# Optimization experiments

Measured on AMD Instinct MI355X. Metric: run time of the kernel, lower is better.

## Reference

```python
import jax, jax.numpy as jnp
import numpy as np

N, E, F, H = 50000, 1600000, 128, 128  # nodes, edges, input_nf, hidden_nf


def setup_inputs() -> dict:
    key = jax.random.key(0)
    ks = jax.random.split(key, 16)
    s = 0.05
    inp = {
        "h": jax.random.normal(ks[0], (N, F), jnp.float32),
        "coord": jax.random.normal(ks[1], (N, 3), jnp.float32),
        "edge_index": jax.random.randint(ks[2], (2, E), 0, N, jnp.int32),
        # edge_mlp: Linear(2F+1, H) -> SiLU -> Linear(H, H) -> SiLU
        "We1": jax.random.normal(ks[3], (2 * F + 1, H), jnp.float32) * s,
        "be1": jnp.zeros((H,), jnp.float32),
        "We2": jax.random.normal(ks[4], (H, H), jnp.float32) * s,
        "be2": jnp.zeros((H,), jnp.float32),
        # node_mlp: Linear(H+F, H) -> SiLU -> Linear(H, F)
        "Wn1": jax.random.normal(ks[5], (H + F, H), jnp.float32) * s,
        "bn1": jnp.zeros((H,), jnp.float32),
        "Wn2": jax.random.normal(ks[6], (H, F), jnp.float32) * s,
        "bn2": jnp.zeros((F,), jnp.float32),
        # coord_mlp: Linear(H, H) -> SiLU -> Linear(H, 1, bias=False) (xavier gain 0.001)
        "Wc1": jax.random.normal(ks[7], (H, H), jnp.float32) * s,
        "bc1": jnp.zeros((H,), jnp.float32),
        "Wc2": jax.random.normal(ks[8], (H, 1), jnp.float32) * 0.001,
    }
    return inp


def reference(h, coord, edge_index, We1, be1, We2, be2, Wn1, bn1, Wn2, bn2, Wc1, bc1, Wc2):
    row, col = edge_index[0], edge_index[1]
    n = h.shape[0]

    # coord2radial (normalize=False)
    coord_diff = coord[row] - coord[col]                      # [E, 3]
    radial = jnp.sum(coord_diff * coord_diff, axis=1, keepdims=True)  # [E, 1]

    # edge_model (attention=False, edge_attr=None)
    e_in = jnp.concatenate([h[row], h[col], radial], axis=1)  # [E, 2F+1]
    edge_feat = jax.nn.silu(jax.nn.silu(e_in @ We1 + be1) @ We2 + be2)  # [E, H]

    # coord_model (coords_agg='mean', reflection_equiv=True, tanh=False)
    phi = jax.nn.silu(edge_feat @ Wc1 + bc1) @ Wc2            # [E, 1]
    trans = coord_diff * phi                                   # [E, 3]
    agg_c = jax.ops.segment_sum(trans, row, num_segments=n)    # [N, 3]
    cnt = jax.ops.segment_sum(jnp.ones((trans.shape[0], 1), trans.dtype), row, num_segments=n)
    coord_out = coord + agg_c / jnp.maximum(cnt, 1.0)

    # node_model (node_attr=None, residual=True)
    agg_h = jax.ops.segment_sum(edge_feat, row, num_segments=n)  # [N, H]
    n_in = jnp.concatenate([h, agg_h], axis=1)                   # [N, F+H]
    h_out = h + (jax.nn.silu(n_in @ Wn1 + bn1) @ Wn2 + bn2)

    return h_out, coord_out
```

## Files before the change

### kernel.cpp

```cpp
#include <hip/hip_runtime.h>


typedef float f32x4 __attribute__((ext_vector_type(4)));
typedef short s16x8 __attribute__((ext_vector_type(8)));

#define NN   50000
#define EE   1600000
#define NHF  6400000
#define NBIN 50000
#define NT   25000
#define A1B  782
#define NODB 782

__device__ __forceinline__ unsigned short f2bf(float x){
  union { float f; unsigned int u; } v; v.f = x;
  unsigned int r = v.u + 0x7fffu + ((v.u >> 16) & 1u);
  return (unsigned short)(r >> 16);
}
__device__ __forceinline__ unsigned int pack2(float a, float b){
  unsigned int r;
  asm("v_cvt_pk_bf16_f32 %0, %1, %2" : "=v"(r) : "v"(a), "v"(b));
  return r;
}
__device__ __forceinline__ float silu_f(float x){
  return x * __builtin_amdgcn_rcpf(1.f + __expf(-x));
}
__device__ __forceinline__ float bflo(unsigned int u){ return __uint_as_float(u << 16); }
__device__ __forceinline__ float bfhi(unsigned int u){ return __uint_as_float(u & 0xffff0000u); }

__device__ __forceinline__ f32x4 mfma16(s16x8 a, s16x8 b, f32x4 c){
  return __builtin_amdgcn_mfma_f32_16x16x32_bf16(a, b, c, 0, 0, 0);
}

template<int CTRL> __device__ __forceinline__ float dppf(float x){
  return __int_as_float(__builtin_amdgcn_update_dpp(0, __float_as_int(x), CTRL, 0xF, 0xF, true));
}
template<int CTRL> __device__ __forceinline__ int dppi(int x){
  return __builtin_amdgcn_update_dpp(-1, x, CTRL, 0xF, 0xF, false);
}

__device__ __forceinline__ short* sptr(short* base, int fi, int slot){
  return (short*)((char*)base + (fi << 10) + (((slot << 4) ^ ((fi & 3) << 5))));
}

__global__ void pack_weights(const float* __restrict__ We1, const float* __restrict__ We2,
                             const float* __restrict__ Wc1, const float* __restrict__ Wn1,
                             const float* __restrict__ Wn2, short* __restrict__ wp)
{
  int b = blockIdx.x;
  int m = b >> 5, t = b & 31;
  int ft = t >> 2, ks = t & 3;
  int lane = threadIdx.x;
  const float* src;
  switch (m) {
    case 0: src = We1;            break;
    case 1: src = We1 + 128*128;  break;
    case 2: src = We2;            break;
    case 3: src = Wc1;            break;
    case 4: src = Wn1;            break;
    case 5: src = Wn1 + 128*128;  break;
    default: src = Wn2;           break;
  }
  short* dst = wp + m*16384 + (((ft<<2) + ks)*64 + lane)*8;
  int f  = (ft<<4) + (lane & 15);
  int kb = (ks<<5) + ((lane >> 4) << 3);
#pragma unroll
  for (int j = 0; j < 8; ++j)
    dst[j] = (short)f2bf(src[(kb + j)*128 + f]);
}

__global__ __launch_bounds__(256, 2)
void a1hist_kernel(const float* __restrict__ h32, const short* __restrict__ wp,
                   const float* __restrict__ be1, const float* __restrict__ bn1,
                   unsigned short* __restrict__ A1,
                   const int* __restrict__ eidx, int* __restrict__ hist)
{
  if (blockIdx.x >= A1B) {
    int e = (blockIdx.x - A1B)*256 + threadIdx.x;
    if (e < EE) atomicAdd(&hist[eidx[e]], 1);
    return;
  }
  __shared__ short sA[16][64][8];
  const int tid = threadIdx.x, w = tid >> 6, lane = tid & 63;
  const int n0 = blockIdx.x << 6;
  const int el = tid >> 2, q = tid & 3;
  const int fi0 = ((el >> 4) << 2) + q, er = el & 15;
  {
    const int node = n0 + el;
    if (node < NN) {
      const float* hp = h32 + (size_t)node*128 + q*32;
#pragma unroll
      for (int lg = 0; lg < 4; ++lg) {
        f32x4 u = *(const f32x4*)(hp + lg*8);
        f32x4 v = *(const f32x4*)(hp + lg*8 + 4);
        uint4 o;
        o.x = pack2(u.x, u.y); o.y = pack2(u.z, u.w);
        o.z = pack2(v.x, v.y); o.w = pack2(v.z, v.w);
        *(uint4*)&sA[fi0][lg*16 + er][0] = o;
      }
    } else {
      s16x8 z = {};
#pragma unroll
      for (int lg = 0; lg < 4; ++lg) *(s16x8*)&sA[fi0][lg*16 + er][0] = z;
    }
  }
  __syncthreads();

  static const int wpm[3] = {0, 1, 4};
#pragma unroll
  for (int p = 0; p < 2; ++p) {
    s16x8 af[3][4];
#pragma unroll
    for (int j = 0; j < 3; ++j) {
      const int ftg = w*6 + p*3 + j;
      const int mi = ftg >> 3, fti = ftg & 7;
#pragma unroll
      for (int ks = 0; ks < 4; ++ks)
        af[j][ks] = *(const s16x8*)(wp + wpm[mi]*16384 + (((fti<<2) + ks)*64 + lane)*8);
    }
    f32x4 acc[3][4] = {};
#pragma unroll
    for (int et = 0; et < 4; ++et)
#pragma unroll
      for (int ks = 0; ks < 4; ++ks) {
        s16x8 b = *(const s16x8*)&sA[et*4+ks][lane][0];
#pragma unroll
        for (int j = 0; j < 3; ++j)
          acc[j][et] = mfma16(af[j][ks], b, acc[j][et]);
      }
#pragma unroll
    for (int j = 0; j < 3; ++j) {
      const int ftg = w*6 + p*3 + j;
      const int mi = ftg >> 3, fti = ftg & 7;
      const int obase = mi*128 + ((fti >> 1) << 5) + ((fti & 1) << 2);
      const int ftrue = (fti << 4) + ((lane >> 4) << 2);
      f32x4 bia = {0.f, 0.f, 0.f, 0.f};
      if (mi == 0) bia = *(const f32x4*)(be1 + ftrue);
      else if (mi == 2) bia = *(const f32x4*)(bn1 + ftrue);
#pragma unroll
      for (int et = 0; et < 4; ++et) {
        const int node = n0 + et*16 + (lane & 15);
        if (node < NN) {
          f32x4 a = acc[j][et];
          uint2 o; o.x = pack2(a.x + bia.x, a.y + bia.y);
          o.y = pack2(a.z + bia.z, a.w + bia.w);
          *(uint2*)(A1 + (size_t)node*384 + obase + ((lane >> 4) << 3)) = o;
        }
      }
    }
  }
}

__global__ void scanA(const int* __restrict__ hist, int* __restrict__ cur,
                      int* __restrict__ btot)
{
  __shared__ int s[256];
  const int t = threadIdx.x;
  const int i = blockIdx.x*256 + t;
  int v = (i < NBIN) ? hist[i] : 0;
  s[t] = v; __syncthreads();
  int acc = v;
#pragma unroll
  for (int d = 1; d < 256; d <<= 1) {
    int u = (t >= d) ? s[t - d] : 0;
    __syncthreads();
    acc += u; s[t] = acc;
    __syncthreads();
  }
  if (i < NBIN) cur[i] = acc - v;
  if (t == 255) btot[blockIdx.x] = acc;
}
__global__ void scanB(int* __restrict__ btot)
{
  __shared__ int s[256];
  const int t = threadIdx.x;
  int v = (t < 196) ? btot[t] : 0;
  s[t] = v; __syncthreads();
  int acc = v;
#pragma unroll
  for (int d = 1; d < 256; d <<= 1) {
    int u = (t >= d) ? s[t - d] : 0;
    __syncthreads();
    acc += u; s[t] = acc;
    __syncthreads();
  }
  if (t < 196) btot[t] = acc - v;
}

__global__ void scatter_k(const int* __restrict__ eidx, int* __restrict__ cur,
                          const int* __restrict__ btot, const float* __restrict__ coord,
                          int2* __restrict__ rc, float* __restrict__ cdr)
{
  int e = blockIdx.x*256 + threadIdx.x;
  if (e < EE) {
    int r = eidx[e], c = eidx[EE + e];
    int p = atomicAdd(&cur[r], 1) + btot[r >> 8];
    int2 v; v.x = r; v.y = c;
    rc[p] = v;
    float dx = coord[3*r+0] - coord[3*c+0];
    float dy = coord[3*r+1] - coord[3*c+1];
    float dz = coord[3*r+2] - coord[3*c+2];
    f32x4 o; o.x = dx; o.y = dy; o.z = dz; o.w = dx*dx + dy*dy + dz*dz;
    *(f32x4*)(cdr + 4*(size_t)p) = o;
  }
}

__global__ __launch_bounds__(256, 4)
void edge_kernel(const unsigned short* __restrict__ A1, const float* __restrict__ cdr,
                 const int2* __restrict__ rc, const short* __restrict__ wp,
                 const float* __restrict__ be2, const float* __restrict__ bc1,
                 const float* __restrict__ We1, const float* __restrict__ Wc2,
                 float* __restrict__ aggh, float* __restrict__ aggc,
                 float* __restrict__ cntb)
{
  __shared__ short sAf[2][16*64*8];
  __shared__ float s_vec[4][128];
  __shared__ float s_phi[64];

  const int tid  = threadIdx.x;
  const int w    = tid >> 6, lane = tid & 63;
  const int ecol = lane & 15, rgrp = lane >> 4;

  if (tid < 128) {
    s_vec[0][tid] = be2[tid];
    s_vec[1][tid] = bc1[tid];
    s_vec[2][tid] = We1[256*128 + tid];
    s_vec[3][tid] = Wc2[tid];
  }

  s16x8 wf2[2][4], wf3[2][4];
#pragma unroll
  for (int f2 = 0; f2 < 2; ++f2)
#pragma unroll
    for (int ks = 0; ks < 4; ++ks) {
      wf2[f2][ks] = *(const s16x8*)(wp + 2*16384 + ((((2*w+f2)<<2) + ks)*64 + lane)*8);
      wf3[f2][ks] = *(const s16x8*)(wp + 3*16384 + ((((2*w+f2)<<2) + ks)*64 + lane)*8);
    }
  __syncthreads();

  short* sb0 = &sAf[0][0];
  short* sb1 = &sAf[1][0];

  const int tbeg = blockIdx.x * 13;
  const int tend = (tbeg + 13 < NT) ? tbeg + 13 : NT;
  const int gbase = (w << 5) + (rgrp << 3);

  for (int t = tbeg; t < tend; ++t) {
    const int e0 = t << 6;

    int rr[4], cc[4]; float rd[4];
#pragma unroll
    for (int et = 0; et < 4; ++et) {
      int2 v = rc[e0 + et*16 + ecol];
      rr[et] = v.x; cc[et] = v.y;
      rd[et] = cdr[4*(size_t)(e0 + et*16 + ecol) + 3];
    }
    if (tid < 64) s_phi[tid] = 0.f;

    {
      uint4 gr4[4], gc4[4];
#pragma unroll
      for (int et = 0; et < 4; ++et) {
        gr4[et] = *(const uint4*)(A1 + (size_t)rr[et]*384 + gbase);
        gc4[et] = *(const uint4*)(A1 + (size_t)cc[et]*384 + 128 + gbase);
      }
#pragma unroll
      for (int f2 = 0; f2 < 2; ++f2) {
        const int f0 = (2*w+f2)*16 + (rgrp << 2);
        const int ks2 = f0 >> 5, lg2 = (f0 & 31) >> 3, j0 = f0 & 7;
        f32x4 w1c = *(const f32x4*)&s_vec[2][f0];
#pragma unroll
        for (int et = 0; et < 4; ++et) {
          uint2 rv, cv;
          rv.x = f2 ? gr4[et].z : gr4[et].x;
          rv.y = f2 ? gr4[et].w : gr4[et].y;
          cv.x = f2 ? gc4[et].z : gc4[et].x;
          cv.y = f2 ? gc4[et].w : gc4[et].y;
          f32x4 x;
          x.x = silu_f(bflo(rv.x) + bflo(cv.x) + rd[et]*w1c.x);
          x.y = silu_f(bfhi(rv.x) + bfhi(cv.x) + rd[et]*w1c.y);
          x.z = silu_f(bflo(rv.y) + bflo(cv.y) + rd[et]*w1c.z);
          x.w = silu_f(bfhi(rv.y) + bfhi(cv.y) + rd[et]*w1c.w);
          uint2 p; p.x = pack2(x.x, x.y); p.y = pack2(x.z, x.w);
          *(uint2*)((char*)sptr(sb0, et*4 + ks2, lg2*16 + ecol) + 2*j0) = p;
        }
      }
    }
    __syncthreads();

    f32x4 a2[2][4] = {};
#pragma unroll
    for (int et = 0; et < 4; ++et)
#pragma unroll
      for (int ks = 0; ks < 4; ++ks) {
        s16x8 b = *(const s16x8*)sptr(sb0, et*4+ks, lane);
        a2[0][et] = mfma16(wf2[0][ks], b, a2[0][et]);
        a2[1][et] = mfma16(wf2[1][ks], b, a2[1][et]);
      }
#pragma unroll
    for (int et = 0; et < 4; ++et) {
      const int r_l = rr[et];
      f32x4 xx0, xx1;
#pragma unroll
      for (int f2 = 0; f2 < 2; ++f2) {
        const int f0 = (2*w+f2)*16 + (rgrp << 2);
        const int ks2 = f0 >> 5, lg2 = (f0 & 31) >> 3, j0 = f0 & 7;
        f32x4 b2 = *(const f32x4*)&s_vec[0][f0];
        f32x4 x = a2[f2][et];
        x.x = silu_f(x.x + b2.x); x.y = silu_f(x.y + b2.y);
        x.z = silu_f(x.z + b2.z); x.w = silu_f(x.w + b2.w);
        uint2 p; p.x = pack2(x.x, x.y); p.y = pack2(x.z, x.w);
        *(uint2*)((char*)sptr(sb1, et*4 + ks2, lg2*16 + ecol) + 2*j0) = p;
        if (f2 == 0) xx0 = x; else xx1 = x;
      }
#define SEG_ROUND(CTRL) { \
      int rn = dppi<CTRL>(r_l); \
      float m = (rn == r_l) ? 1.f : 0.f; \
      xx0.x += dppf<CTRL>(xx0.x)*m; \
      xx0.y += dppf<CTRL>(xx0.y)*m; \
      xx0.z += dppf<CTRL>(xx0.z)*m; \
      xx0.w += dppf<CTRL>(xx0.w)*m; \
      xx1.x += dppf<CTRL>(xx1.x)*m; \
      xx1.y += dppf<CTRL>(xx1.y)*m; \
      xx1.z += dppf<CTRL>(xx1.z)*m; \
      xx1.w += dppf<CTRL>(xx1.w)*m; }
      SEG_ROUND(0x101)
      SEG_ROUND(0x102)
      SEG_ROUND(0x104)
      SEG_ROUND(0x108)
#undef SEG_ROUND
      const int rprev = dppi<0x111>(r_l);
      if (rprev != r_l) {
        const int f0a = (2*w+0)*16 + (rgrp << 2);
        const int f0b = (2*w+1)*16 + (rgrp << 2);
        float* aga = aggh + (size_t)r_l*128 + f0a;
        float* agb = aggh + (size_t)r_l*128 + f0b;
        atomicAdd(aga+0, xx0.x); atomicAdd(aga+1, xx0.y);
        atomicAdd(aga+2, xx0.z); atomicAdd(aga+3, xx0.w);
        atomicAdd(agb+0, xx1.x); atomicAdd(agb+1, xx1.y);
        atomicAdd(agb+2, xx1.z); atomicAdd(agb+3, xx1.w);
      }
    }
    __syncthreads();

    f32x4 a3[2][4] = {};
#pragma unroll
    for (int et = 0; et < 4; ++et)
#pragma unroll
      for (int ks = 0; ks < 4; ++ks) {
        s16x8 b = *(const s16x8*)sptr(sb1, et*4+ks, lane);
        a3[0][et] = mfma16(wf3[0][ks], b, a3[0][et]);
        a3[1][et] = mfma16(wf3[1][ks], b, a3[1][et]);
      }
#pragma unroll
    for (int et = 0; et < 4; ++et) {
      float p = 0.f;
#pragma unroll
      for (int f2 = 0; f2 < 2; ++f2) {
        const int f0 = (2*w+f2)*16 + (rgrp << 2);
        f32x4 bc = *(const f32x4*)&s_vec[1][f0];
        f32x4 wc = *(const f32x4*)&s_vec[3][f0];
        f32x4 x = a3[f2][et];
        p += silu_f(x.x + bc.x)*wc.x + silu_f(x.y + bc.y)*wc.y
           + silu_f(x.z + bc.z)*wc.z + silu_f(x.w + bc.w)*wc.w;
      }
      p += __shfl_xor(p, 16);
      p += __shfl_xor(p, 32);
      if (rgrp == 0) atomicAdd(&s_phi[et*16 + ecol], p);
    }
    __syncthreads();

    if (tid < 64) {
      int2 v = rc[e0 + tid];
      int r = v.x;
      f32x4 cd = *(const f32x4*)(cdr + 4*(size_t)(e0 + tid));
      float ph = s_phi[tid];
      float cx = cd.x*ph, cy = cd.y*ph, cz = cd.z*ph, c1 = 1.f;
#pragma unroll
      for (int d = 1; d < 64; d <<= 1) {
        const int sl = tid + d;
        int   r2 = __shfl(r,  sl, 64);
        float ux = __shfl(cx, sl, 64), uy = __shfl(cy, sl, 64);
        float uz = __shfl(cz, sl, 64), uw = __shfl(c1, sl, 64);
        if ((sl < 64) && (r2 == r)) { cx+=ux; cy+=uy; cz+=uz; c1+=uw; }
      }
      const int rp = __shfl(r, tid - 1, 64);
      if (tid == 0 || rp != r) {
        atomicAdd(&aggc[3*r+0], cx); atomicAdd(&aggc[3*r+1], cy);
        atomicAdd(&aggc[3*r+2], cz); atomicAdd(&cntb[r], c1);
      }
    }
  }
}

__global__ __launch_bounds__(256, 2)
void nodecoord_kernel(const unsigned short* __restrict__ A1, const float* __restrict__ h32,
                      const short* __restrict__ wp, const float* __restrict__ bn2,
                      const float* __restrict__ coord, const float* __restrict__ aggc,
                      const float* __restrict__ cntb, float* __restrict__ hout)
{
  if (blockIdx.x >= NODB) {
    int i = (blockIdx.x - NODB)*256 + threadIdx.x;
    if (i < NN) {
      float inv = __builtin_amdgcn_rcpf(fmaxf(cntb[i], 1.f));
      hout[NHF + 3*i+0] = coord[3*i+0] + aggc[3*i+0]*inv;
      hout[NHF + 3*i+1] = coord[3*i+1] + aggc[3*i+1]*inv;
      hout[NHF + 3*i+2] = coord[3*i+2] + aggc[3*i+2]*inv;
    }
    return;
  }
  __shared__ short sA[16][64][8];
  __shared__ float s_vec[128];
  const int tid  = threadIdx.x, w = tid >> 6, lane = tid & 63;
  const int ecol = lane & 15, rgrp = lane >> 4;
  if (tid < 128) s_vec[tid] = bn2[tid];

  s16x8 wfa[2][4], wfb[2][4];
#pragma unroll
  for (int f2 = 0; f2 < 2; ++f2)
#pragma unroll
    for (int ks = 0; ks < 4; ++ks) {
      wfa[f2][ks] = *(const s16x8*)(wp + 5*16384 + ((((2*w+f2)<<2) + ks)*64 + lane)*8);
      wfb[f2][ks] = *(const s16x8*)(wp + 6*16384 + ((((2*w+f2)<<2) + ks)*64 + lane)*8);
    }

  const int n0 = blockIdx.x << 6;
  const int el = tid >> 2, q = tid & 3;
  const int fi0 = ((el >> 4) << 2) + q, er = el & 15;
  {
    const int node = n0 + el;
    if (node < NN) {
      const float* ap = hout + (size_t)node*128 + q*32;
#pragma unroll
      for (int lg = 0; lg < 4; ++lg) {
        f32x4 u = *(const f32x4*)(ap + lg*8);
        f32x4 v = *(const f32x4*)(ap + lg*8 + 4);
        uint4 o;
        o.x = pack2(u.x, u.y); o.y = pack2(u.z, u.w);
        o.z = pack2(v.x, v.y); o.w = pack2(v.z, v.w);
        *(uint4*)&sA[fi0][lg*16 + er][0] = o;
      }
    } else {
      s16x8 z = {};
#pragma unroll
      for (int lg = 0; lg < 4; ++lg) *(s16x8*)&sA[fi0][lg*16 + er][0] = z;
    }
  }
  __syncthreads();

  f32x4 acc[2][4] = {};
#pragma unroll
  for (int et = 0; et < 4; ++et)
#pragma unroll
    for (int ks = 0; ks < 4; ++ks) {
      s16x8 ba = *(const s16x8*)&sA[et*4+ks][lane][0];
      acc[0][et] = mfma16(wfa[0][ks], ba, acc[0][et]);
      acc[1][et] = mfma16(wfa[1][ks], ba, acc[1][et]);
    }
  __syncthreads();

  uint4 g4[4];
  {
    const int gb = 256 + (w << 5) + (rgrp << 3);
#pragma unroll
    for (int et = 0; et < 4; ++et) {
      const int node = n0 + et*16 + ecol;
      if (node < NN) g4[et] = *(const uint4*)(A1 + (size_t)node*384 + gb);
      else { g4[et].x = 0u; g4[et].y = 0u; g4[et].z = 0u; g4[et].w = 0u; }
    }
  }
#pragma unroll
  for (int f2 = 0; f2 < 2; ++f2) {
    const int ft = 2*w + f2, f0 = ft*16 + (rgrp << 2);
    const int ks2 = f0 >> 5, lg2 = (f0 & 31) >> 3, j0 = f0 & 7;
#pragma unroll
    for (int et = 0; et < 4; ++et) {
      uint2 g;
      g.x = f2 ? g4[et].z : g4[et].x;
      g.y = f2 ? g4[et].w : g4[et].y;
      f32x4 x = acc[f2][et];
      x.x = silu_f(x.x + bflo(g.x));
      x.y = silu_f(x.y + bfhi(g.x));
      x.z = silu_f(x.z + bflo(g.y));
      x.w = silu_f(x.w + bfhi(g.y));
      uint2 p; p.x = pack2(x.x, x.y); p.y = pack2(x.z, x.w);
      *(uint2*)&sA[et*4 + ks2][lg2*16 + ecol][j0] = p;
    }
  }
  __syncthreads();

  f32x4 a2[2][4] = {};
#pragma unroll
  for (int et = 0; et < 4; ++et)
#pragma unroll
    for (int ks = 0; ks < 4; ++ks) {
      s16x8 b = *(const s16x8*)&sA[et*4+ks][lane][0];
      a2[0][et] = mfma16(wfb[0][ks], b, a2[0][et]);
      a2[1][et] = mfma16(wfb[1][ks], b, a2[1][et]);
    }
#pragma unroll
  for (int f2 = 0; f2 < 2; ++f2) {
    const int f0 = (2*w+f2)*16 + (rgrp << 2);
    f32x4 b2 = *(const f32x4*)&s_vec[f0];
#pragma unroll
    for (int et = 0; et < 4; ++et) {
      const int node = n0 + et*16 + ecol;
      if (node < NN) {
        f32x4 hv = *(const f32x4*)(h32 + (size_t)node*128 + f0);
        f32x4 x = a2[f2][et];
        x.x += b2.x + hv.x; x.y += b2.y + hv.y;
        x.z += b2.z + hv.z; x.w += b2.w + hv.w;
        *(f32x4*)(hout + (size_t)node*128 + f0) = x;
      }
    }
  }
}

extern "C" void kernel_launch(void* const* d_in, const int* in_sizes, int n_in,
                              void* d_out, int out_size, void* d_ws, size_t ws_size,
                              hipStream_t stream)
{
  (void)in_sizes; (void)n_in; (void)out_size; (void)ws_size;
  const float* h    = (const float*)d_in[0];
  const float* crd  = (const float*)d_in[1];
  const int*   eidx = (const int*)  d_in[2];
  const float* We1  = (const float*)d_in[3];
  const float* be1  = (const float*)d_in[4];
  const float* We2  = (const float*)d_in[5];
  const float* be2  = (const float*)d_in[6];
  const float* Wn1  = (const float*)d_in[7];
  const float* bn1  = (const float*)d_in[8];
  const float* Wn2  = (const float*)d_in[9];
  const float* bn2  = (const float*)d_in[10];
  const float* Wc1  = (const float*)d_in[11];
  const float* bc1  = (const float*)d_in[12];
  const float* Wc2  = (const float*)d_in[13];
  float* out = (float*)d_out;
  char*  ws  = (char*)d_ws;

  short*          wp   = (short*)ws;
  unsigned short* A1   = (unsigned short*)(ws + 229376);
  float*          aggc = (float*)(ws + 38629376);
  float*          cntb = (float*)(ws + 39229376);
  int*            hist = (int*)  (ws + 39429376);
  int*            cur  = (int*)  (ws + 39629376);
  int*            btot = (int*)  (ws + 39829376);
  int2*           rc   = (int2*) (ws + 39830400);
  float*          cdr  = (float*)(ws + 52630400);

  hipMemsetAsync(out, 0, (size_t)NHF*4, stream);
  hipMemsetAsync(ws + 38629376, 0, 800000, stream);
  hipMemsetAsync(ws + 39429376, 0, 200000, stream);

  pack_weights<<<dim3(224), dim3(64), 0, stream>>>(We1, We2, Wc1, Wn1, Wn2, wp);
  a1hist_kernel<<<dim3(A1B + 6250), dim3(256), 0, stream>>>(h, wp, be1, bn1, A1, eidx, hist);
  scanA<<<dim3(196), dim3(256), 0, stream>>>(hist, cur, btot);
  scanB<<<dim3(1), dim3(256), 0, stream>>>(btot);
  scatter_k<<<dim3(6250), dim3(256), 0, stream>>>(eidx, cur, btot, crd, rc, cdr);
  edge_kernel<<<dim3(1924), dim3(256), 0, stream>>>(A1, cdr, rc, wp,
                                                    be2, bc1, We1, Wc2,
                                                    out, aggc, cntb);
  nodecoord_kernel<<<dim3(NODB + 196), dim3(256), 0, stream>>>(A1, h, wp, bn2,
                                                               crd, aggc, cntb, out);
}
```

Before: 704.7 us.

## Split edge kernel work across eight waves with one feature tile each

```diff
diff --git a/kernel.cpp b/kernel.cpp
--- a/kernel.cpp
+++ b/kernel.cpp
@@ -205,7 +205,7 @@
   }
 }
 
-__global__ __launch_bounds__(256, 4)
+__global__ __launch_bounds__(512, 4)
 void edge_kernel(const unsigned short* __restrict__ A1, const float* __restrict__ cdr,
                  const int2* __restrict__ rc, const short* __restrict__ wp,
                  const float* __restrict__ be2, const float* __restrict__ bc1,
@@ -228,22 +228,27 @@
     s_vec[3][tid] = Wc2[tid];
   }
 
-  s16x8 wf2[2][4], wf3[2][4];
-#pragma unroll
-  for (int f2 = 0; f2 < 2; ++f2)
-#pragma unroll
-    for (int ks = 0; ks < 4; ++ks) {
-      wf2[f2][ks] = *(const s16x8*)(wp + 2*16384 + ((((2*w+f2)<<2) + ks)*64 + lane)*8);
-      wf3[f2][ks] = *(const s16x8*)(wp + 3*16384 + ((((2*w+f2)<<2) + ks)*64 + lane)*8);
-    }
+  s16x8 wf2[4], wf3[4];
+#pragma unroll
+  for (int ks = 0; ks < 4; ++ks) {
+    wf2[ks] = *(const s16x8*)(wp + 2*16384 + (((w<<2) + ks)*64 + lane)*8);
+    wf3[ks] = *(const s16x8*)(wp + 3*16384 + (((w<<2) + ks)*64 + lane)*8);
+  }
   __syncthreads();
+
+  const int f0  = (w << 4) + (rgrp << 2);
+  const int ks2 = f0 >> 5, lg2 = (f0 & 31) >> 3, j0 = f0 & 7;
+  const int ga  = ((w >> 1) << 5) + (rgrp << 3) + ((w & 1) << 2);
+  const f32x4 w1c = *(const f32x4*)&s_vec[2][f0];
+  const f32x4 b2v = *(const f32x4*)&s_vec[0][f0];
+  const f32x4 bcv = *(const f32x4*)&s_vec[1][f0];
+  const f32x4 wcv = *(const f32x4*)&s_vec[3][f0];
 
   short* sb0 = &sAf[0][0];
   short* sb1 = &sAf[1][0];
 
   const int tbeg = blockIdx.x * 13;
   const int tend = (tbeg + 13 < NT) ? tbeg + 13 : NT;
-  const int gbase = (w << 5) + (rgrp << 3);
 
   for (int t = tbeg; t < tend; ++t) {
     const int e0 = t << 6;
@@ -258,72 +263,50 @@
     if (tid < 64) s_phi[tid] = 0.f;
 
     {
-      uint4 gr4[4], gc4[4];
+      uint2 gr2[4], gc2[4];
 #pragma unroll
       for (int et = 0; et < 4; ++et) {
-        gr4[et] = *(const uint4*)(A1 + (size_t)rr[et]*384 + gbase);
-        gc4[et] = *(const uint4*)(A1 + (size_t)cc[et]*384 + 128 + gbase);
-      }
-#pragma unroll
-      for (int f2 = 0; f2 < 2; ++f2) {
-        const int f0 = (2*w+f2)*16 + (rgrp << 2);
-        const int ks2 = f0 >> 5, lg2 = (f0 & 31) >> 3, j0 = f0 & 7;
-        f32x4 w1c = *(const f32x4*)&s_vec[2][f0];
-#pragma unroll
-        for (int et = 0; et < 4; ++et) {
-          uint2 rv, cv;
-          rv.x = f2 ? gr4[et].z : gr4[et].x;
-          rv.y = f2 ? gr4[et].w : gr4[et].y;
-          cv.x = f2 ? gc4[et].z : gc4[et].x;
-          cv.y = f2 ? gc4[et].w : gc4[et].y;
-          f32x4 x;
-          x.x = silu_f(bflo(rv.x) + bflo(cv.x) + rd[et]*w1c.x);
-          x.y = silu_f(bfhi(rv.x) + bfhi(cv.x) + rd[et]*w1c.y);
-          x.z = silu_f(bflo(rv.y) + bflo(cv.y) + rd[et]*w1c.z);
-          x.w = silu_f(bfhi(rv.y) + bfhi(cv.y) + rd[et]*w1c.w);
-          uint2 p; p.x = pack2(x.x, x.y); p.y = pack2(x.z, x.w);
-          *(uint2*)((char*)sptr(sb0, et*4 + ks2, lg2*16 + ecol) + 2*j0) = p;
-        }
-      }
-    }
-    __syncthreads();
-
-    f32x4 a2[2][4] = {};
+        gr2[et] = *(const uint2*)(A1 + (size_t)rr[et]*384 + ga);
+        gc2[et] = *(const uint2*)(A1 + (size_t)cc[et]*384 + 128 + ga);
+      }
+#pragma unroll
+      for (int et = 0; et < 4; ++et) {
+        const uint2 rv = gr2[et], cv = gc2[et];
+        f32x4 x;
+        x.x = silu_f(bflo(rv.x) + bflo(cv.x) + rd[et]*w1c.x);
+        x.y = silu_f(bfhi(rv.x) + bfhi(cv.x) + rd[et]*w1c.y);
+        x.z = silu_f(bflo(rv.y) + bflo(cv.y) + rd[et]*w1c.z);
+        x.w = silu_f(bfhi(rv.y) + bfhi(cv.y) + rd[et]*w1c.w);
+        uint2 p; p.x = pack2(x.x, x.y); p.y = pack2(x.z, x.w);
+        *(uint2*)((char*)sptr(sb0, et*4 + ks2, lg2*16 + ecol) + 2*j0) = p;
+      }
+    }
+    __syncthreads();
+
+    f32x4 a2[4] = {};
 #pragma unroll
     for (int et = 0; et < 4; ++et)
 #pragma unroll
       for (int ks = 0; ks < 4; ++ks) {
         s16x8 b = *(const s16x8*)sptr(sb0, et*4+ks, lane);
-        a2[0][et] = mfma16(wf2[0][ks], b, a2[0][et]);
-        a2[1][et] = mfma16(wf2[1][ks], b, a2[1][et]);
+        a2[et] = mfma16(wf2[ks], b, a2[et]);
       }
 #pragma unroll
     for (int et = 0; et < 4; ++et) {
       const int r_l = rr[et];
-      f32x4 xx0, xx1;
-#pragma unroll
-      for (int f2 = 0; f2 < 2; ++f2) {
-        const int f0 = (2*w+f2)*16 + (rgrp << 2);
-        const int ks2 = f0 >> 5, lg2 = (f0 & 31) >> 3, j0 = f0 & 7;
-        f32x4 b2 = *(const f32x4*)&s_vec[0][f0];
-        f32x4 x = a2[f2][et];
-        x.x = silu_f(x.x + b2.x); x.y = silu_f(x.y + b2.y);
-        x.z = silu_f(x.z + b2.z); x.w = silu_f(x.w + b2.w);
-        uint2 p; p.x = pack2(x.x, x.y); p.y = pack2(x.z, x.w);
-        *(uint2*)((char*)sptr(sb1, et*4 + ks2, lg2*16 + ecol) + 2*j0) = p;
-        if (f2 == 0) xx0 = x; else xx1 = x;
-      }
+      f32x4 x = a2[et];
+      x.x = silu_f(x.x + b2v.x); x.y = silu_f(x.y + b2v.y);
+      x.z = silu_f(x.z + b2v.z); x.w = silu_f(x.w + b2v.w);
+      uint2 p; p.x = pack2(x.x, x.y); p.y = pack2(x.z, x.w);
+      *(uint2*)((char*)sptr(sb1, et*4 + ks2, lg2*16 + ecol) + 2*j0) = p;
+      f32x4 xx = x;
 #define SEG_ROUND(CTRL) { \
       int rn = dppi<CTRL>(r_l); \
       float m = (rn == r_l) ? 1.f : 0.f; \
-      xx0.x += dppf<CTRL>(xx0.x)*m; \
-      xx0.y += dppf<CTRL>(xx0.y)*m; \
-      xx0.z += dppf<CTRL>(xx0.z)*m; \
-      xx0.w += dppf<CTRL>(xx0.w)*m; \
-      xx1.x += dppf<CTRL>(xx1.x)*m; \
-      xx1.y += dppf<CTRL>(xx1.y)*m; \
-      xx1.z += dppf<CTRL>(xx1.z)*m; \
-      xx1.w += dppf<CTRL>(xx1.w)*m; }
+      xx.x += dppf<CTRL>(xx.x)*m; \
+      xx.y += dppf<CTRL>(xx.y)*m; \
+      xx.z += dppf<CTRL>(xx.z)*m; \
+      xx.w += dppf<CTRL>(xx.w)*m; }
       SEG_ROUND(0x101)
       SEG_ROUND(0x102)
       SEG_ROUND(0x104)
@@ -331,39 +314,26 @@
 #undef SEG_ROUND
       const int rprev = dppi<0x111>(r_l);
       if (rprev != r_l) {
-        const int f0a = (2*w+0)*16 + (rgrp << 2);
-        const int f0b = (2*w+1)*16 + (rgrp << 2);
-        float* aga = aggh + (size_t)r_l*128 + f0a;
-        float* agb = aggh + (size_t)r_l*128 + f0b;
-        atomicAdd(aga+0, xx0.x); atomicAdd(aga+1, xx0.y);
-        atomicAdd(aga+2, xx0.z); atomicAdd(aga+3, xx0.w);
-        atomicAdd(agb+0, xx1.x); atomicAdd(agb+1, xx1.y);
-        atomicAdd(agb+2, xx1.z); atomicAdd(agb+3, xx1.w);
-      }
-    }
-    __syncthreads();
-
-    f32x4 a3[2][4] = {};
+        float* ag = aggh + (size_t)r_l*128 + f0;
+        atomicAdd(ag+0, xx.x); atomicAdd(ag+1, xx.y);
+        atomicAdd(ag+2, xx.z); atomicAdd(ag+3, xx.w);
+      }
+    }
+    __syncthreads();
+
+    f32x4 a3[4] = {};
 #pragma unroll
     for (int et = 0; et < 4; ++et)
 #pragma unroll
       for (int ks = 0; ks < 4; ++ks) {
         s16x8 b = *(const s16x8*)sptr(sb1, et*4+ks, lane);
-        a3[0][et] = mfma16(wf3[0][ks], b, a3[0][et]);
-        a3[1][et] = mfma16(wf3[1][ks], b, a3[1][et]);
+        a3[et] = mfma16(wf3[ks], b, a3[et]);
       }
 #pragma unroll
     for (int et = 0; et < 4; ++et) {
-      float p = 0.f;
-#pragma unroll
-      for (int f2 = 0; f2 < 2; ++f2) {
-        const int f0 = (2*w+f2)*16 + (rgrp << 2);
-        f32x4 bc = *(const f32x4*)&s_vec[1][f0];
-        f32x4 wc = *(const f32x4*)&s_vec[3][f0];
-        f32x4 x = a3[f2][et];
-        p += silu_f(x.x + bc.x)*wc.x + silu_f(x.y + bc.y)*wc.y
-           + silu_f(x.z + bc.z)*wc.z + silu_f(x.w + bc.w)*wc.w;
-      }
+      f32x4 x = a3[et];
+      float p = silu_f(x.x + bcv.x)*wcv.x + silu_f(x.y + bcv.y)*wcv.y
+              + silu_f(x.z + bcv.z)*wcv.z + silu_f(x.w + bcv.w)*wcv.w;
       p += __shfl_xor(p, 16);
       p += __shfl_xor(p, 32);
       if (rgrp == 0) atomicAdd(&s_phi[et*16 + ecol], p);
@@ -557,7 +527,7 @@
   scanA<<<dim3(196), dim3(256), 0, stream>>>(hist, cur, btot);
   scanB<<<dim3(1), dim3(256), 0, stream>>>(btot);
   scatter_k<<<dim3(6250), dim3(256), 0, stream>>>(eidx, cur, btot, crd, rc, cdr);
-  edge_kernel<<<dim3(1924), dim3(256), 0, stream>>>(A1, cdr, rc, wp,
+  edge_kernel<<<dim3(1924), dim3(512), 0, stream>>>(A1, cdr, rc, wp,
                                                     be2, bc1, We1, Wc2,
                                                     out, aggc, cntb);
   nodecoord_kernel<<<dim3(NODB + 196), dim3(256), 0, stream>>>(A1, h, wp, bn2,
```

New measurement: 692.4 us. About the same (-1.7%).
